# Optimization experiments

Hardware: AMD Instinct MI355X
Metric: run time of the kernel (lower is better)

## Reference

```python
import jax, jax.numpy as jnp
import numpy as np

N, M, D_IN, H1, D, OUT_C = 2048, 128, 352, 512, 256, 13


def _lin_bn_relu(x, w, b, g, be):
    # 1x1 conv == linear over last dim; BN (eval) folded to per-channel affine (g, be)
    return jax.nn.relu(g * (x @ w.T + b) + be)


def _encode(x, wA, bA, gA, beA, wB, bB, gB, beB):
    return _lin_bn_relu(_lin_bn_relu(x, wA, bA, gA, beA), wB, bB, gB, beB)


def setup_inputs() -> dict:
    key = jax.random.key(0)
    ks = iter(jax.random.split(key, 64))

    def wgt(shape, s=0.05):
        return (jax.random.normal(next(ks), shape, jnp.float32) * s)

    def gamma(c):
        return 1.0 + 0.05 * jax.random.normal(next(ks), (c,), jnp.float32)

    inp = {}
    inp['ext_fea'] = jax.random.normal(next(ks), (N, D_IN), jnp.float32)
    inp['lab_fea'] = jax.random.normal(next(ks), (M, D_IN), jnp.float32)
    # convs1: 352->512->256, each Conv1d(1x1)+BN+ReLU
    inp.update(w1a=wgt((H1, D_IN)), b1a=wgt((H1,)), g1a=gamma(H1), be1a=wgt((H1,)))
    inp.update(w1b=wgt((D, H1)), b1b=wgt((D,)), g1b=gamma(D), be1b=wgt((D,)))
    # convs2: same shapes
    inp.update(w2a=wgt((H1, D_IN)), b2a=wgt((H1,)), g2a=gamma(H1), be2a=wgt((H1,)))
    inp.update(w2b=wgt((D, H1)), b2b=wgt((D,)), g2b=gamma(D), be2b=wgt((D,)))
    # wei_conv SharedMLP [256,32,64,256]: three Conv2d(1x1)+BN+ReLU
    inp.update(mw1=wgt((32, D)), mb1=wgt((32,)), mg1=gamma(32), mbe1=wgt((32,)))
    inp.update(mw2=wgt((64, 32)), mb2=wgt((64,)), mg2=gamma(64), mbe2=wgt((64,)))
    inp.update(mw3=wgt((D, 64)), mb3=wgt((D,)), mg3=gamma(D), mbe3=wgt((D,)))
    # fc
    inp.update(fcw=wgt((OUT_C, D)), fcb=wgt((OUT_C,)))
    return inp


def reference(ext_fea, lab_fea,
              w1a, b1a, g1a, be1a, w1b, b1b, g1b, be1b,
              w2a, b2a, g2a, be2a, w2b, b2b, g2b, be2b,
              mw1, mb1, mg1, mbe1, mw2, mb2, mg2, mbe2, mw3, mb3, mg3, mbe3,
              fcw, fcb):
    A = _encode(ext_fea, w1a, b1a, g1a, be1a, w1b, b1b, g1b, be1b)   # [N, 256]
    B = _encode(lab_fea, w2a, b2a, g2a, be2a, w2b, b2b, g2b, be2b)   # [M, 256]
    diff = A[:, None, :] - B[None, :, :]                             # [N, M, 256]
    h = _lin_bn_relu(diff, mw1, mb1, mg1, mbe1)                      # [N, M, 32]
    h = _lin_bn_relu(h, mw2, mb2, mg2, mbe2)                         # [N, M, 64]
    wei = _lin_bn_relu(h, mw3, mb3, mg3, mbe3)                       # [N, M, 256]
    # torch softmax over dim=-1 of [1,256,N,M] == over M == axis 1 here
    wei = jax.nn.softmax(wei, axis=1)
    att = jnp.sum(wei * diff, axis=1)                                # [N, 256]
    return att @ fcw.T + fcb                                         # [N, 13]
```

## Files before the change

### kernel.cpp

```cpp
#include <hip/hip_runtime.h>
#include <stdint.h>


typedef __attribute__((ext_vector_type(4))) float float4_t;
typedef __attribute__((ext_vector_type(4))) float f32x4;
typedef __attribute__((ext_vector_type(8))) short bf16x8;
typedef __attribute__((ext_vector_type(8))) unsigned short ushort8_t;
typedef __attribute__((ext_vector_type(4))) unsigned short ushort4_t;
typedef unsigned short ushort_t;

__device__ __forceinline__ float b2f(unsigned short u) {
  union { unsigned int i; float f; } v; v.i = ((unsigned int)u) << 16; return v.f;
}
__device__ __forceinline__ unsigned short f2b(float f) {
  union { float f; unsigned int i; } v; v.f = f;
  unsigned int x = v.i;
  return (unsigned short)((x + 0x7FFFu + ((x >> 16) & 1u)) >> 16);
}

template<int ISBF>
__device__ __forceinline__ ushort8_t ld8(const void* base, size_t idx) {
  if constexpr (ISBF) {
    return *(const ushort8_t*)((const ushort_t*)base + idx);
  } else {
    const float* p = (const float*)base + idx;
    float4_t v0 = *(const float4_t*)p;
    float4_t v1 = *(const float4_t*)(p + 4);
    ushort8_t u;
    #pragma unroll
    for (int e = 0; e < 4; ++e) { u[e] = f2b(v0[e]); u[4 + e] = f2b(v1[e]); }
    return u;
  }
}

template<int XBF, int WBF, int OUT_BF16>
__global__ __launch_bounds__(256) void enc_mfma(
    const void* __restrict__ XA, const void* __restrict__ WA,
    const float* __restrict__ bA, const float* __restrict__ gA, const float* __restrict__ beA,
    void* __restrict__ YA,
    const void* __restrict__ XB, const void* __restrict__ WB,
    const float* __restrict__ bB, const float* __restrict__ gB, const float* __restrict__ beB,
    void* __restrict__ YB, ushort_t* __restrict__ YBTb,
    int J, int K, int nbxA)
{
  __shared__ ushort_t Xs[2][32][40];
  __shared__ ushort_t Ws[2][32][40];
  const int bx = blockIdx.x, by = blockIdx.y;
  const void* X; const void* W;
  const float *bb, *gg, *bev; void* Y; int i0, isB;
  if (bx < nbxA) { X = XA; W = WA; bb = bA; gg = gA; bev = beA; Y = YA; i0 = bx * 32; isB = 0; }
  else           { X = XB; W = WB; bb = bB; gg = gB; bev = beB; Y = YB; i0 = (bx - nbxA) * 32; isB = 1; }
  const int j0 = by * 32;
  const int tid = threadIdx.x, w = tid >> 6, lane = tid & 63, lg = lane >> 4, lr = lane & 15;
  const int mt = w >> 1, ct = w & 1;
  const int row = tid >> 2, k8 = (tid & 3) * 8;

  f32x4 acc = f32x4{0.f, 0.f, 0.f, 0.f};

  ushort8_t sv = (row < 32) ? ld8<XBF>(X, (size_t)(i0 + row) * K + k8)
                            : ld8<WBF>(W, (size_t)(j0 + row - 32) * K + k8);
  for (int kt = 0; kt < K; kt += 32) {
    const int buf = (kt >> 5) & 1;
    if (row < 32) *(ushort8_t*)&Xs[buf][row][k8] = sv;
    else          *(ushort8_t*)&Ws[buf][row - 32][k8] = sv;
    __syncthreads();
    if (kt + 32 < K)
      sv = (row < 32) ? ld8<XBF>(X, (size_t)(i0 + row) * K + kt + 32 + k8)
                      : ld8<WBF>(W, (size_t)(j0 + row - 32) * K + kt + 32 + k8);
    bf16x8 af = *(const bf16x8*)&Xs[buf][mt * 16 + lr][lg * 8];
    bf16x8 bf_ = *(const bf16x8*)&Ws[buf][ct * 16 + lr][lg * 8];
    acc = __builtin_amdgcn_mfma_f32_16x16x32_bf16(af, bf_, acc, 0, 0, 0);
  }
  const int c = j0 + ct * 16 + lr;
  const float g = gg[c], bv = bb[c], ev = bev[c];
  #pragma unroll
  for (int r = 0; r < 4; ++r) {
    const int rowo = i0 + mt * 16 + 4 * lg + r;
    float t = fmaxf(g * (acc[r] + bv) + ev, 0.f);
    if (OUT_BF16) ((ushort_t*)Y)[(size_t)rowo * J + c] = f2b(t);
    else {
      ((float*)Y)[(size_t)rowo * J + c] = t;
      if (isB && YBTb) YBTb[(size_t)c * 128 + rowo] = f2b(t);
    }
  }
}

__global__ __launch_bounds__(256) void proj32(
    const float* __restrict__ Aenc, const float* __restrict__ Benc,
    const float* __restrict__ mw1, const float* __restrict__ mb1,
    const float* __restrict__ mg1, const float* __restrict__ mbe1,
    float* __restrict__ PA2, float* __restrict__ PB2, int nbxA,
    const float* __restrict__ mw2, const float* __restrict__ mw3,
    ushort_t* __restrict__ mw2b, ushort_t* __restrict__ mw3b)
{
  __shared__ float ps[4][32];
  const int tid = threadIdx.x, bx = blockIdx.x;
  if (bx >= nbxA + 32) {
    const int g = (bx - nbxA - 32) * 256 + tid;
    const float* s; ushort_t* d; int j;
    if (g < 256) { s = mw2; d = mw2b; j = g; }
    else         { s = mw3; d = mw3b; j = g - 256; }
    float4_t v0 = *(const float4_t*)&s[(size_t)j * 8];
    float4_t v1 = *(const float4_t*)&s[(size_t)j * 8 + 4];
    ushort8_t u;
    #pragma unroll
    for (int e = 0; e < 4; ++e) { u[e] = f2b(v0[e]); u[4 + e] = f2b(v1[e]); }
    *(ushort8_t*)&d[(size_t)j * 8] = u;
    return;
  }
  const float* X; float* P; int n0, wb;
  if (bx < nbxA) { X = Aenc; P = PA2; n0 = bx * 4; wb = 1; }
  else           { X = Benc; P = PB2; n0 = (bx - nbxA) * 4; wb = 0; }
  const int k = tid & 31, r = (tid >> 5) & 3, half = tid >> 7;
  const int n = n0 + r;
  const float* xp = &X[(size_t)n * 256 + half * 128];
  const float* wp = &mw1[k * 256 + half * 128];
  float s = 0.f;
  #pragma unroll 8
  for (int q = 0; q < 128; q += 4) {
    float4_t xv = *(const float4_t*)&xp[q];
    float4_t wv = *(const float4_t*)&wp[q];
    #pragma unroll
    for (int e = 0; e < 4; ++e) s = fmaf(xv[e], wv[e], s);
  }
  if (half == 1) ps[r][k] = s;
  __syncthreads();
  if (half == 0) {
    s += ps[r][k];
    P[(size_t)n * 32 + k] = wb ? (mg1[k] * (s + mb1[k]) + mbe1[k]) : (mg1[k] * s);
  }
}

__global__ __launch_bounds__(256, 3) void main_attn(
    const float* __restrict__ PA2, const float* __restrict__ PB2,
    const float* __restrict__ A, const ushort_t* __restrict__ BmTb,
    const ushort_t* __restrict__ mw2b, const float* __restrict__ mb2,
    const float* __restrict__ mg2, const float* __restrict__ mbe2,
    const ushort_t* __restrict__ mw3b, const float* __restrict__ mb3,
    const float* __restrict__ mg3, const float* __restrict__ mbe3,
    const float* __restrict__ fcw, const float* __restrict__ fcb,
    float* __restrict__ outp)
{
  __shared__ __align__(16) char smem[36864];
  const int tid = threadIdx.x;
  const int w = tid >> 6, lane = tid & 63, lg = lane >> 4, lr = lane & 15;
  const int n = blockIdx.x * 4 + w;
  ushort_t* h2f = (ushort_t*)(smem + w * 9216);
  float* attL   = (float*)(smem + w * 9216 + 8192);
  const float LOG2E = 1.4426950408889634f;

  bf16x8 b1[4];
  float g2h[4], c2h[4];
  #pragma unroll
  for (int jt = 0; jt < 4; ++jt) {
    b1[jt] = *(const bf16x8*)&mw2b[(jt * 16 + lr) * 32 + lg * 8];
    const int j = jt * 16 + lr;
    const float g = mg2[j];
    g2h[jt] = g; c2h[jt] = g * mb2[j] + mbe2[j];
  }
  const float* pa = &PA2[(size_t)n * 32 + lg * 8];
  float4_t pa0 = *(const float4_t*)pa;
  float4_t pa1 = *(const float4_t*)(pa + 4);

  float smv[16], wbv[16];
  #pragma unroll
  for (int ct = 0; ct < 16; ++ct) { smv[ct] = 0.f; wbv[ct] = 0.f; }

  #pragma unroll 1
  for (int half = 0; half < 2; ++half) {
    #pragma unroll
    for (int mt = 0; mt < 4; ++mt) {
      const int m = half * 64 + mt * 16 + lr;
      const float* pb = &PB2[(size_t)m * 32 + lg * 8];
      float4_t pb0 = *(const float4_t*)pb;
      float4_t pb1 = *(const float4_t*)(pb + 4);
      bf16x8 a1;
      #pragma unroll
      for (int e = 0; e < 4; ++e) {
        a1[e]     = (short)f2b(fmaxf(pa0[e] - pb0[e], 0.f));
        a1[4 + e] = (short)f2b(fmaxf(pa1[e] - pb1[e], 0.f));
      }
      f32x4 acc1[4];
      #pragma unroll
      for (int jt = 0; jt < 4; ++jt) acc1[jt] = f32x4{0.f, 0.f, 0.f, 0.f};
      #pragma unroll
      for (int jt = 0; jt < 4; ++jt)
        acc1[jt] = __builtin_amdgcn_mfma_f32_16x16x32_bf16(a1, b1[jt], acc1[jt], 0, 0, 0);
      #pragma unroll
      for (int jt = 0; jt < 4; ++jt) {
        const int ks = jt >> 1;
        const int lg_r = ((jt & 1) << 1) | (lr >> 3);
        const int e = lr & 7;
        const int base = (mt * 8 + ks * 4 + lg_r) * 128 + e;
        #pragma unroll
        for (int r = 0; r < 4; ++r)
          h2f[base + (4 * lg + r) * 8] =
              f2b(fmaxf(fmaf(g2h[jt], acc1[jt][r], c2h[jt]), 0.f));
      }
    }

    #pragma unroll 4
    for (int ct = 0; ct < 16; ++ct) {
      const int c = ct * 16 + lr;
      bf16x8 bfr0 = *(const bf16x8*)&mw3b[(size_t)c * 64 + lg * 8];
      bf16x8 bfr1 = *(const bf16x8*)&mw3b[(size_t)c * 64 + 32 + lg * 8];
      f32x4 acc[4];
      #pragma unroll
      for (int mt = 0; mt < 4; ++mt) acc[mt] = f32x4{0.f, 0.f, 0.f, 0.f};
      #pragma unroll
      for (int mt = 0; mt < 4; ++mt) {
        bf16x8 af0 = *(const bf16x8*)&h2f[(mt * 8 + lg) * 128 + lr * 8];
        acc[mt] = __builtin_amdgcn_mfma_f32_16x16x32_bf16(af0, bfr0, acc[mt], 0, 0, 0);
        bf16x8 af1 = *(const bf16x8*)&h2f[(mt * 8 + 4 + lg) * 128 + lr * 8];
        acc[mt] = __builtin_amdgcn_mfma_f32_16x16x32_bf16(af1, bfr1, acc[mt], 0, 0, 0);
      }
      const float g = mg3[c];
      const float gs = g * LOG2E;
      const float cs = (g * mb3[c] + mbe3[c]) * LOG2E;
      f32x4 sm4 = f32x4{0.f, 0.f, 0.f, 0.f};
      f32x4 wb4 = f32x4{0.f, 0.f, 0.f, 0.f};
      #pragma unroll
      for (int mt = 0; mt < 4; ++mt) {
        ushort4_t bv4 = *(const ushort4_t*)&BmTb[(size_t)c * 128 + half * 64 + mt * 16 + 4 * lg];
        #pragma unroll
        for (int r = 0; r < 4; ++r) {
          float t = fmaf(gs, acc[mt][r], cs);
          float p = __builtin_amdgcn_exp2f(__builtin_amdgcn_fmed3f(t, 0.f, 80.f));
          sm4[r] += p;
          wb4[r] = fmaf(p, b2f(bv4[r]), wb4[r]);
        }
      }
      smv[ct] += (sm4[0] + sm4[1]) + (sm4[2] + sm4[3]);
      wbv[ct] += (wb4[0] + wb4[1]) + (wb4[2] + wb4[3]);
    }
  }

  #pragma unroll
  for (int ct = 0; ct < 16; ++ct) {
    float sm = smv[ct], wb = wbv[ct];
    sm += __shfl_xor(sm, 16, 64);  wb += __shfl_xor(wb, 16, 64);
    sm += __shfl_xor(sm, 32, 64);  wb += __shfl_xor(wb, 32, 64);
    if (lg == 0) {
      const int c = ct * 16 + lr;
      attL[c] = A[(size_t)n * 256 + c] - wb / sm;
    }
  }

  {
    float4_t av = *(const float4_t*)&attL[lane * 4];
    #pragma unroll
    for (int o = 0; o < 13; ++o) {
      float4_t wv = *(const float4_t*)&fcw[(size_t)o * 256 + lane * 4];
      float s = av[0] * wv[0];
      s = fmaf(av[1], wv[1], s);
      s = fmaf(av[2], wv[2], s);
      s = fmaf(av[3], wv[3], s);
      #pragma unroll
      for (int st = 1; st <= 32; st <<= 1) s += __shfl_xor(s, st, 64);
      if (lane == 0) outp[(size_t)n * 13 + o] = s + fcb[o];
    }
  }
}

extern "C" void kernel_launch(void* const* d_in, const int* in_sizes, int n_in,
                              void* d_out, int out_size, void* d_ws, size_t ws_size,
                              hipStream_t stream)
{
  const float* ext = (const float*)d_in[0];
  const float* lab = (const float*)d_in[1];
  const float* w1a = (const float*)d_in[2];
  const float* b1a = (const float*)d_in[3];
  const float* g1a = (const float*)d_in[4];
  const float* be1a= (const float*)d_in[5];
  const float* w1b = (const float*)d_in[6];
  const float* b1b = (const float*)d_in[7];
  const float* g1b = (const float*)d_in[8];
  const float* be1b= (const float*)d_in[9];
  const float* w2a = (const float*)d_in[10];
  const float* b2a = (const float*)d_in[11];
  const float* g2a = (const float*)d_in[12];
  const float* be2a= (const float*)d_in[13];
  const float* w2b = (const float*)d_in[14];
  const float* b2b = (const float*)d_in[15];
  const float* g2b = (const float*)d_in[16];
  const float* be2b= (const float*)d_in[17];
  const float* mw1 = (const float*)d_in[18];
  const float* mb1 = (const float*)d_in[19];
  const float* mg1 = (const float*)d_in[20];
  const float* mbe1= (const float*)d_in[21];
  const float* mw2 = (const float*)d_in[22];
  const float* mb2 = (const float*)d_in[23];
  const float* mg2 = (const float*)d_in[24];
  const float* mbe2= (const float*)d_in[25];
  const float* mw3 = (const float*)d_in[26];
  const float* mb3 = (const float*)d_in[27];
  const float* mg3 = (const float*)d_in[28];
  const float* mbe3= (const float*)d_in[29];
  const float* fcw = (const float*)d_in[30];
  const float* fcb = (const float*)d_in[31];

  char* ws = (char*)d_ws;
  ushort_t* Y1ab = (ushort_t*)(ws);
  float*    PA2  = (float*)(ws);
  float*    PB2  = (float*)(ws + 262144);
  float*    Aenc = (float*)(ws + (2u << 20));
  char* b5 = ws + (4u << 20);
  ushort_t* mw2b  = (ushort_t*)(b5);
  ushort_t* mw3b  = (ushort_t*)(b5 + 4096);
  ushort_t* Y1bb  = (ushort_t*)(b5 + 36864);
  float*    Benc  = (float*)(b5 + 167936);
  ushort_t* BencTb= (ushort_t*)(b5 + 299008);

  enc_mfma<0, 0, 1><<<dim3(68, 16), 256, 0, stream>>>(
      (const void*)ext, (const void*)w1a, b1a, g1a, be1a, (void*)Y1ab,
      (const void*)lab, (const void*)w2a, b2a, g2a, be2a, (void*)Y1bb,
      (ushort_t*)nullptr, 512, 352, 64);
  enc_mfma<1, 0, 0><<<dim3(68, 8), 256, 0, stream>>>(
      (const void*)Y1ab, (const void*)w1b, b1b, g1b, be1b, (void*)Aenc,
      (const void*)Y1bb, (const void*)w2b, b2b, g2b, be2b, (void*)Benc,
      BencTb, 256, 512, 64);
  proj32<<<553, 256, 0, stream>>>(Aenc, Benc, mw1, mb1, mg1, mbe1, PA2, PB2, 512,
                                  mw2, mw3, mw2b, mw3b);
  main_attn<<<512, 256, 0, stream>>>(PA2, PB2, Aenc, BencTb,
                                     mw2b, mb2, mg2, mbe2, mw3b, mb3, mg3, mbe3,
                                     fcw, fcb, (float*)d_out);
}
```

Before: 96.30 us.

## Split main attention per row across waves by channel, fold BN2 scale into weights

Each block now handles one output row, and its four waves split the 256 channels into 64-channel quarters. Before, each wave processed a full row. Each wave recomputes the layer-2 MLP for its row, now with the BN gamma folded into the bf16 weights and the bias preloaded into the MFMA accumulator. The layer-2 output is transposed through a small double-buffered LDS scratch into register fragments, and the BN3 constants are precomputed in proj32. This cuts per-wave register and LDS footprint so occupancy can rise to four blocks per SIMD, at the cost of computing the layer-2 MLP four times per row and adding block syncs for the FC reduction.

```diff
diff --git a/kernel.cpp b/kernel.cpp
--- a/kernel.cpp
+++ b/kernel.cpp
@@ -91,21 +91,40 @@
     const float* __restrict__ mg1, const float* __restrict__ mbe1,
     float* __restrict__ PA2, float* __restrict__ PB2, int nbxA,
     const float* __restrict__ mw2, const float* __restrict__ mw3,
-    ushort_t* __restrict__ mw2b, ushort_t* __restrict__ mw3b)
+    const float* __restrict__ mg2, const float* __restrict__ mb2, const float* __restrict__ mbe2,
+    const float* __restrict__ mg3, const float* __restrict__ mb3, const float* __restrict__ mbe3,
+    ushort_t* __restrict__ mw2bs, ushort_t* __restrict__ mw3b,
+    float* __restrict__ c2arr, float* __restrict__ gs3arr, float* __restrict__ cs3arr)
 {
   __shared__ float ps[4][32];
   const int tid = threadIdx.x, bx = blockIdx.x;
+  const float LOG2E = 1.4426950408889634f;
   if (bx >= nbxA + 32) {
-    const int g = (bx - nbxA - 32) * 256 + tid;
-    const float* s; ushort_t* d; int j;
-    if (g < 256) { s = mw2; d = mw2b; j = g; }
-    else         { s = mw3; d = mw3b; j = g - 256; }
-    float4_t v0 = *(const float4_t*)&s[(size_t)j * 8];
-    float4_t v1 = *(const float4_t*)&s[(size_t)j * 8 + 4];
-    ushort8_t u;
-    #pragma unroll
-    for (int e = 0; e < 4; ++e) { u[e] = f2b(v0[e]); u[4 + e] = f2b(v1[e]); }
-    *(ushort8_t*)&d[(size_t)j * 8] = u;
+    const int t = bx - nbxA - 32;
+    if (t == 9) {
+      if (tid < 64)  c2arr[tid] = mg2[tid] * mb2[tid] + mbe2[tid];
+      gs3arr[tid] = mg3[tid] * LOG2E;
+      cs3arr[tid] = (mg3[tid] * mb3[tid] + mbe3[tid]) * LOG2E;
+      return;
+    }
+    const int g = t * 256 + tid;
+    if (g < 256) {
+      const float sc = mg2[g >> 2];
+      float4_t v0 = *(const float4_t*)&mw2[(size_t)g * 8];
+      float4_t v1 = *(const float4_t*)&mw2[(size_t)g * 8 + 4];
+      ushort8_t u;
+      #pragma unroll
+      for (int e = 0; e < 4; ++e) { u[e] = f2b(sc * v0[e]); u[4 + e] = f2b(sc * v1[e]); }
+      *(ushort8_t*)&mw2bs[(size_t)g * 8] = u;
+    } else {
+      const int j = g - 256;
+      float4_t v0 = *(const float4_t*)&mw3[(size_t)j * 8];
+      float4_t v1 = *(const float4_t*)&mw3[(size_t)j * 8 + 4];
+      ushort8_t u;
+      #pragma unroll
+      for (int e = 0; e < 4; ++e) { u[e] = f2b(v0[e]); u[4 + e] = f2b(v1[e]); }
+      *(ushort8_t*)&mw3b[(size_t)j * 8] = u;
+    }
     return;
   }
   const float* X; float* P; int n0, wb;
@@ -131,43 +150,54 @@
   }
 }
 
-__global__ __launch_bounds__(256, 3) void main_attn(
+__global__ __launch_bounds__(256, 4) void main_attn(
     const float* __restrict__ PA2, const float* __restrict__ PB2,
     const float* __restrict__ A, const ushort_t* __restrict__ BmTb,
-    const ushort_t* __restrict__ mw2b, const float* __restrict__ mb2,
-    const float* __restrict__ mg2, const float* __restrict__ mbe2,
-    const ushort_t* __restrict__ mw3b, const float* __restrict__ mb3,
-    const float* __restrict__ mg3, const float* __restrict__ mbe3,
+    const ushort_t* __restrict__ mw2bs, const float* __restrict__ c2arr,
+    const ushort_t* __restrict__ mw3b, const float* __restrict__ gs3arr,
+    const float* __restrict__ cs3arr,
     const float* __restrict__ fcw, const float* __restrict__ fcb,
     float* __restrict__ outp)
 {
-  __shared__ __align__(16) char smem[36864];
+  __shared__ __align__(16) char smem[20288];
   const int tid = threadIdx.x;
   const int w = tid >> 6, lane = tid & 63, lg = lane >> 4, lr = lane & 15;
-  const int n = blockIdx.x * 4 + w;
-  ushort_t* h2f = (ushort_t*)(smem + w * 9216);
-  float* attL   = (float*)(smem + w * 9216 + 8192);
-  const float LOG2E = 1.4426950408889634f;
-
-  bf16x8 b1[4];
-  float g2h[4], c2h[4];
-  #pragma unroll
-  for (int jt = 0; jt < 4; ++jt) {
-    b1[jt] = *(const bf16x8*)&mw2b[(jt * 16 + lr) * 32 + lg * 8];
-    const int j = jt * 16 + lr;
-    const float g = mg2[j];
-    g2h[jt] = g; c2h[jt] = g * mb2[j] + mbe2[j];
+  const int n = blockIdx.x;
+  const int cbase = w * 64;
+  ushort_t* scrA = (ushort_t*)(smem + w * 4608);
+  ushort_t* scrB = scrA + 1152;
+  float* attL = (float*)(smem + 18432);
+  float* part = (float*)(smem + 19456);
+
+  float c2v[16];
+  #pragma unroll
+  for (int jt = 0; jt < 4; ++jt)
+    #pragma unroll
+    for (int r = 0; r < 4; ++r)
+      c2v[jt * 4 + r] = c2arr[jt * 16 + 4 * lg + r];
+  float gs3[4], cs3[4];
+  #pragma unroll
+  for (int ct = 0; ct < 4; ++ct) {
+    const int c = cbase + ct * 16 + lr;
+    gs3[ct] = gs3arr[c];
+    cs3[ct] = cs3arr[c];
   }
   const float* pa = &PA2[(size_t)n * 32 + lg * 8];
   float4_t pa0 = *(const float4_t*)pa;
   float4_t pa1 = *(const float4_t*)(pa + 4);
 
-  float smv[16], wbv[16];
-  #pragma unroll
-  for (int ct = 0; ct < 16; ++ct) { smv[ct] = 0.f; wbv[ct] = 0.f; }
+  float smv[4], wbv[4];
+  #pragma unroll
+  for (int ct = 0; ct < 4; ++ct) { smv[ct] = 0.f; wbv[ct] = 0.f; }
 
   #pragma unroll 1
   for (int half = 0; half < 2; ++half) {
+    bf16x8 b1[4];
+    #pragma unroll
+    for (int jt = 0; jt < 4; ++jt)
+      b1[jt] = *(const bf16x8*)&mw2bs[(jt * 16 + lr) * 32 + lg * 8];
+
+    bf16x8 af0[4], af1[4];
     #pragma unroll
     for (int mt = 0; mt < 4; ++mt) {
       const int m = half * 64 + mt * 16 + lr;
@@ -182,26 +212,28 @@
       }
       f32x4 acc1[4];
       #pragma unroll
-      for (int jt = 0; jt < 4; ++jt) acc1[jt] = f32x4{0.f, 0.f, 0.f, 0.f};
-      #pragma unroll
       for (int jt = 0; jt < 4; ++jt)
-        acc1[jt] = __builtin_amdgcn_mfma_f32_16x16x32_bf16(a1, b1[jt], acc1[jt], 0, 0, 0);
+        acc1[jt] = f32x4{c2v[jt * 4 + 0], c2v[jt * 4 + 1], c2v[jt * 4 + 2], c2v[jt * 4 + 3]};
+      #pragma unroll
+      for (int jt = 0; jt < 4; ++jt)
+        acc1[jt] = __builtin_amdgcn_mfma_f32_16x16x32_bf16(b1[jt], a1, acc1[jt], 0, 0, 0);
+      ushort_t* scr = (mt & 1) ? scrB : scrA;
       #pragma unroll
       for (int jt = 0; jt < 4; ++jt) {
-        const int ks = jt >> 1;
-        const int lg_r = ((jt & 1) << 1) | (lr >> 3);
-        const int e = lr & 7;
-        const int base = (mt * 8 + ks * 4 + lg_r) * 128 + e;
-        #pragma unroll
-        for (int r = 0; r < 4; ++r)
-          h2f[base + (4 * lg + r) * 8] =
-              f2b(fmaxf(fmaf(g2h[jt], acc1[jt][r], c2h[jt]), 0.f));
-      }
-    }
-
-    #pragma unroll 4
-    for (int ct = 0; ct < 16; ++ct) {
-      const int c = ct * 16 + lr;
+        unsigned int lo = (unsigned int)f2b(fmaxf(acc1[jt][0], 0.f))
+                        | ((unsigned int)f2b(fmaxf(acc1[jt][1], 0.f)) << 16);
+        unsigned int hi = (unsigned int)f2b(fmaxf(acc1[jt][2], 0.f))
+                        | ((unsigned int)f2b(fmaxf(acc1[jt][3], 0.f)) << 16);
+        *(unsigned int*)&scr[lr * 72 + jt * 16 + 4 * lg]     = lo;
+        *(unsigned int*)&scr[lr * 72 + jt * 16 + 4 * lg + 2] = hi;
+      }
+      af0[mt] = *(const bf16x8*)&scr[lr * 72 + lg * 8];
+      af1[mt] = *(const bf16x8*)&scr[lr * 72 + 32 + lg * 8];
+    }
+
+    #pragma unroll
+    for (int ct = 0; ct < 4; ++ct) {
+      const int c = cbase + ct * 16 + lr;
       bf16x8 bfr0 = *(const bf16x8*)&mw3b[(size_t)c * 64 + lg * 8];
       bf16x8 bfr1 = *(const bf16x8*)&mw3b[(size_t)c * 64 + 32 + lg * 8];
       f32x4 acc[4];
@@ -209,14 +241,9 @@
       for (int mt = 0; mt < 4; ++mt) acc[mt] = f32x4{0.f, 0.f, 0.f, 0.f};
       #pragma unroll
       for (int mt = 0; mt < 4; ++mt) {
-        bf16x8 af0 = *(const bf16x8*)&h2f[(mt * 8 + lg) * 128 + lr * 8];
-        acc[mt] = __builtin_amdgcn_mfma_f32_16x16x32_bf16(af0, bfr0, acc[mt], 0, 0, 0);
-        bf16x8 af1 = *(const bf16x8*)&h2f[(mt * 8 + 4 + lg) * 128 + lr * 8];
-        acc[mt] = __builtin_amdgcn_mfma_f32_16x16x32_bf16(af1, bfr1, acc[mt], 0, 0, 0);
-      }
-      const float g = mg3[c];
-      const float gs = g * LOG2E;
-      const float cs = (g * mb3[c] + mbe3[c]) * LOG2E;
+        acc[mt] = __builtin_amdgcn_mfma_f32_16x16x32_bf16(af0[mt], bfr0, acc[mt], 0, 0, 0);
+        acc[mt] = __builtin_amdgcn_mfma_f32_16x16x32_bf16(af1[mt], bfr1, acc[mt], 0, 0, 0);
+      }
       f32x4 sm4 = f32x4{0.f, 0.f, 0.f, 0.f};
       f32x4 wb4 = f32x4{0.f, 0.f, 0.f, 0.f};
       #pragma unroll
@@ -224,7 +251,7 @@
         ushort4_t bv4 = *(const ushort4_t*)&BmTb[(size_t)c * 128 + half * 64 + mt * 16 + 4 * lg];
         #pragma unroll
         for (int r = 0; r < 4; ++r) {
-          float t = fmaf(gs, acc[mt][r], cs);
+          float t = fmaf(gs3[ct], acc[mt][r], cs3[ct]);
           float p = __builtin_amdgcn_exp2f(__builtin_amdgcn_fmed3f(t, 0.f, 80.f));
           sm4[r] += p;
           wb4[r] = fmaf(p, b2f(bv4[r]), wb4[r]);
@@ -236,29 +263,37 @@
   }
 
   #pragma unroll
-  for (int ct = 0; ct < 16; ++ct) {
+  for (int ct = 0; ct < 4; ++ct) {
     float sm = smv[ct], wb = wbv[ct];
     sm += __shfl_xor(sm, 16, 64);  wb += __shfl_xor(wb, 16, 64);
     sm += __shfl_xor(sm, 32, 64);  wb += __shfl_xor(wb, 32, 64);
     if (lg == 0) {
-      const int c = ct * 16 + lr;
+      const int c = cbase + ct * 16 + lr;
       attL[c] = A[(size_t)n * 256 + c] - wb / sm;
     }
   }
+  __syncthreads();
 
   {
-    float4_t av = *(const float4_t*)&attL[lane * 4];
-    #pragma unroll
-    for (int o = 0; o < 13; ++o) {
-      float4_t wv = *(const float4_t*)&fcw[(size_t)o * 256 + lane * 4];
-      float s = av[0] * wv[0];
-      s = fmaf(av[1], wv[1], s);
-      s = fmaf(av[2], wv[2], s);
-      s = fmaf(av[3], wv[3], s);
-      #pragma unroll
-      for (int st = 1; st <= 32; st <<= 1) s += __shfl_xor(s, st, 64);
-      if (lane == 0) outp[(size_t)n * 13 + o] = s + fcb[o];
-    }
+    const int o = tid >> 4, gp = tid & 15;
+    if (o < 13) {
+      float s = 0.f;
+      #pragma unroll
+      for (int i = 0; i < 4; ++i) {
+        float4_t av = *(const float4_t*)&attL[gp * 16 + i * 4];
+        float4_t wv = *(const float4_t*)&fcw[(size_t)o * 256 + gp * 16 + i * 4];
+        #pragma unroll
+        for (int e = 0; e < 4; ++e) s = fmaf(av[e], wv[i == 0 ? e : e], s);
+      }
+      part[o * 16 + gp] = s;
+    }
+  }
+  __syncthreads();
+  if (tid < 13) {
+    float s = fcb[tid];
+    #pragma unroll
+    for (int gp = 0; gp < 16; ++gp) s += part[tid * 16 + gp];
+    outp[(size_t)n * 13 + tid] = s;
   }
 }
 
@@ -305,11 +340,14 @@
   float*    PB2  = (float*)(ws + 262144);
   float*    Aenc = (float*)(ws + (2u << 20));
   char* b5 = ws + (4u << 20);
-  ushort_t* mw2b  = (ushort_t*)(b5);
+  ushort_t* mw2bs = (ushort_t*)(b5);
   ushort_t* mw3b  = (ushort_t*)(b5 + 4096);
   ushort_t* Y1bb  = (ushort_t*)(b5 + 36864);
   float*    Benc  = (float*)(b5 + 167936);
   ushort_t* BencTb= (ushort_t*)(b5 + 299008);
+  float*    c2arr = (float*)(b5 + 364544);
+  float*    gs3arr= (float*)(b5 + 364800);
+  float*    cs3arr= (float*)(b5 + 365824);
 
   enc_mfma<0, 0, 1><<<dim3(68, 16), 256, 0, stream>>>(
       (const void*)ext, (const void*)w1a, b1a, g1a, be1a, (void*)Y1ab,
@@ -319,9 +357,10 @@
       (const void*)Y1ab, (const void*)w1b, b1b, g1b, be1b, (void*)Aenc,
       (const void*)Y1bb, (const void*)w2b, b2b, g2b, be2b, (void*)Benc,
       BencTb, 256, 512, 64);
-  proj32<<<553, 256, 0, stream>>>(Aenc, Benc, mw1, mb1, mg1, mbe1, PA2, PB2, 512,
-                                  mw2, mw3, mw2b, mw3b);
-  main_attn<<<512, 256, 0, stream>>>(PA2, PB2, Aenc, BencTb,
-                                     mw2b, mb2, mg2, mbe2, mw3b, mb3, mg3, mbe3,
-                                     fcw, fcb, (float*)d_out);
-}
+  proj32<<<554, 256, 0, stream>>>(Aenc, Benc, mw1, mb1, mg1, mbe1, PA2, PB2, 512,
+                                  mw2, mw3, mg2, mb2, mbe2, mg3, mb3, mbe3,
+                                  mw2bs, mw3b, c2arr, gs3arr, cs3arr);
+  main_attn<<<2048, 256, 0, stream>>>(PA2, PB2, Aenc, BencTb,
+                                      mw2bs, c2arr, mw3b, gs3arr, cs3arr,
+                                      fcw, fcb, (float*)d_out);
+}
```

New measurement: 123.0 us. +27.7%, slower.
